# Optimization experiments

Measured on AMD Instinct MI355X. Metric: run time of the kernel, lower is better.

Reference implementation:

```python
import jax, jax.numpy as jnp
import numpy as np
import jax.scipy.special as jsp

N_RESERVOIR = 8192
N_INPUT = 64
N_LAYERS = 3
INPUT_SCALE = 0.4
RES_SCALE = 0.9
BIAS_SCALE = 0.1
ALPHA = 1.0  # activation_fn_args = (1.0,)
N_HADAMARD = 1 << int(np.ceil(np.log2(N_INPUT + N_RESERVOIR)))  # 16384
N_PADDING = N_HADAMARD - N_RESERVOIR - N_INPUT
BATCH = 512


def fwht(x):
    """Fast Walsh-Hadamard transform along last axis. x: [B, n], n a power of 2."""
    B, n = x.shape
    h = 1
    while h < n:
        x = x.reshape(B, n // (2 * h), 2, h)
        a = x[:, :, 0, :]
        b = x[:, :, 1, :]
        x = jnp.concatenate([a + b, a - b], axis=-1).reshape(B, n)
        h *= 2
    return x


def leaky_erf(x, state, alpha):
    return (1.0 - alpha) * state + alpha * jsp.erf(x)


def setup_inputs() -> dict:
    key = jax.random.key(0)
    k1, k2, k3, k4 = jax.random.split(key, 4)
    state = jax.random.normal(k1, (BATCH, N_RESERVOIR), dtype=jnp.float32)
    inputs = jax.random.normal(k2, (BATCH, N_INPUT), dtype=jnp.float32)
    bias = BIAS_SCALE * jax.random.normal(k3, (N_RESERVOIR,), dtype=jnp.float32)
    # structured-transform diagonals: random Rademacher signs, one per layer
    diag = jnp.where(jax.random.uniform(k4, (N_LAYERS, N_HADAMARD)) < 0.5, -1.0, 1.0).astype(jnp.float32)
    return {"state": state, "inputs": inputs, "bias": bias, "diag": diag}


def reference(state, inputs, bias, diag):
    B = state.shape[0]
    pad = jnp.zeros((B, N_PADDING), dtype=state.dtype)
    X = jnp.concatenate([RES_SCALE * state, INPUT_SCALE * inputs, pad], axis=1)  # [B, N_HADAMARD]
    for l in range(N_LAYERS):
        X = fwht(X * diag[l])
    z = X[:, :N_RESERVOIR] / N_HADAMARD + bias
    return leaky_erf(z, state, ALPHA)
```

## Files before the change

kernel.cpp:

```cpp
#include <hip/hip_runtime.h>
#include <math.h>

#define NH    16384
#define NRES  8192
#define NINP  64
#define BATCH 512

typedef float v2f __attribute__((ext_vector_type(2)));

__device__ __forceinline__ constexpr int gfoldc(int v) {
    return ((v >> 5) & 7) ^ ((v >> 8) & 7) ^ ((v >> 11) & 7);
}
__device__ __forceinline__ constexpr int physf(int v) { return v ^ (gfoldc(v) << 2); }

template <int T>
__device__ __forceinline__ void pstage(v2f X[32]) {
#pragma unroll
    for (int p = 0; p < 32; ++p) if (!(p & T)) {
        v2f A = X[p], B = X[p | T];
        X[p]     = A + B;
        X[p | T] = A - B;
    }
}
__device__ __forceinline__ void vstage0(v2f X[32]) {
#pragma unroll
    for (int p = 0; p < 32; ++p) {
        float a = X[p].x, b = X[p].y;
        X[p].x = a + b; X[p].y = a - b;
    }
}

template <int CTRL>
__device__ __forceinline__ float dppf(float v) {
    return __builtin_bit_cast(float,
        __builtin_amdgcn_update_dpp(0, __builtin_bit_cast(int, v), CTRL, 0xF, 0xF, true));
}
template <int CTRL>
__device__ __forceinline__ void dpp_bfly(v2f X[32], v2f sgn) {
#pragma unroll
    for (int p = 0; p < 32; ++p) {
        float y0 = dppf<CTRL>(X[p].x);
        float y1 = dppf<CTRL>(X[p].y);
        X[p] = sgn * X[p] + (v2f){y0, y1};
    }
}

__device__ __forceinline__ void pl16_swap(float& a, float& b) {
    asm("v_permlane16_swap_b32 %0, %1" : "+v"(a), "+v"(b));
}
__device__ __forceinline__ void pl32_swap(float& a, float& b) {
    asm("v_permlane32_swap_b32 %0, %1" : "+v"(a), "+v"(b));
}
__device__ __forceinline__ void swap_j2_l4(v2f X[32]) {
#pragma unroll
    for (int p = 0; p < 32; ++p) if (!(p & 8)) {
        float a = X[p].x, b = X[p | 8].x; pl16_swap(a, b); X[p].x = a; X[p | 8].x = b;
        float c = X[p].y, d = X[p | 8].y; pl16_swap(c, d); X[p].y = c; X[p | 8].y = d;
    }
}
__device__ __forceinline__ void swap_j3_l5(v2f X[32]) {
#pragma unroll
    for (int p = 0; p < 32; ++p) if (!(p & 16)) {
        float a = X[p].x, b = X[p | 16].x; pl32_swap(a, b); X[p].x = a; X[p | 16].x = b;
        float c = X[p].y, d = X[p | 16].y; pl32_swap(c, d); X[p].y = c; X[p | 16].y = d;
    }
}

#define GOFF4(g, G0, G1, G2, G3) \
    ((((g) & 1) ? (G0) : 0) | (((g) & 2) ? (G1) : 0) | \
     (((g) & 4) ? (G2) : 0) | (((g) & 8) ? (G3) : 0))

#define WRX(Q, G0, G1, G2, G3) do { _Pragma("unroll") \
    for (int g = 0; g < 16; ++g) { \
        const int a = (Q) ^ physf(GOFF4(g, G0, G1, G2, G3)); \
        lds4[(unsigned)a >> 2] = \
            make_float4(X[2*g].x, X[2*g].y, X[2*g+1].x, X[2*g+1].y); \
    } } while (0)

#define RDX(Q, G0, G1, G2, G3) do { _Pragma("unroll") \
    for (int g = 0; g < 16; ++g) { \
        const int a = (Q) ^ physf(GOFF4(g, G0, G1, G2, G3)); \
        float4 v = lds4[(unsigned)a >> 2]; \
        X[2*g]   = (v2f){v.x, v.y}; \
        X[2*g+1] = (v2f){v.z, v.w}; \
    } } while (0)

#define DIAG_LOAD(PF, BASE, G0, G1, G2, G3) do { _Pragma("unroll") \
    for (int g = 0; g < 16; ++g) \
        (PF)[g] = *(const float4*)((BASE) + GOFF4(g, G0, G1, G2, G3)); } while (0)

#define DIAG_APPLY(PF) do { _Pragma("unroll") \
    for (int g = 0; g < 16; ++g) { \
        X[2*g]   *= (v2f){(PF)[g].x, (PF)[g].y}; \
        X[2*g+1] *= (v2f){(PF)[g].z, (PF)[g].w}; \
    } } while (0)

#define BAR() asm volatile("s_waitcnt lgkmcnt(0)\n\ts_barrier" ::: "memory")

__device__ __forceinline__ float erf_fast(float z) {
    float p = z * z;
    float u = z * fmaf(p, 0.10090f, 1.1283793f);
    float e = __builtin_amdgcn_exp2f(u * 2.8853902f);
    float r = __builtin_amdgcn_rcpf(e + 1.0f);
    return fmaf(-2.0f, r, 1.0f);
}

__global__ __launch_bounds__(256, 2) void st_kernel(
    const float* __restrict__ state, const float* __restrict__ inputs,
    const float* __restrict__ bias,  const float* __restrict__ diag,
    float* __restrict__ out)
{
    __shared__ float4 lds4[NH / 4];
    const int t = threadIdx.x;
    const int r = blockIdx.x;
    const int l = t & 63, w = t >> 6;
    const int l0=l&1, l1=(l>>1)&1, l2=(l>>2)&1, l3=(l>>3)&1, l4=(l>>4)&1, l5=(l>>5)&1;
    const int w0=w&1, w1=(w>>1)&1;

    const v2f s1 = (v2f){l0 ? -1.f : 1.f, l0 ? -1.f : 1.f};
    const v2f s2 = (v2f){l1 ? -1.f : 1.f, l1 ? -1.f : 1.f};

    const int b_w1 = l0*64 + l1*128 + l2*256 + l3*512 + l4*16 + l5*32
                   + w0*4096 + w1*8192;
    const int b_r1 = l0*4 + l1*8 + l2*64 + l3*128 + l4*16 + l5*32
                   + w0*1024 + w1*2048;
    const int b_w2 = l0*4 + l1*8 + l2*64 + l3*128 + l4*4096 + l5*8192
                   + w0*1024 + w1*2048;
    const int b_r2 = l0*4 + l1*8 + l2*256 + l3*512 + l4*16 + l5*32
                   + w0*4096 + w1*8192;
    const int b_w3 = l0*4 + l1*8 + l2*256 + l3*512 + l4*1024 + l5*2048
                   + w0*4096 + w1*8192;

    v2f X[32];
    float4 pf[16];

    if (t < 128) {
        const float* srow = state + (size_t)r * NRES + t * 64;
        const float* d0   = diag + t * 64;
#pragma unroll
        for (int g = 0; g < 16; ++g) {
            float4 v = *(const float4*)(srow + 4 * g);
            float4 d = *(const float4*)(d0 + 4 * g);
            X[2*g]   = (v2f){0.9f * v.x * d.x, 0.9f * v.y * d.y};
            X[2*g+1] = (v2f){0.9f * v.z * d.z, 0.9f * v.w * d.w};
        }
    } else if (t == 128) {
        const float* irow = inputs + r * NINP;
        const float* d0   = diag + NRES;
#pragma unroll
        for (int g = 0; g < 16; ++g) {
            float4 v = *(const float4*)(irow + 4 * g);
            float4 d = *(const float4*)(d0 + 4 * g);
            X[2*g]   = (v2f){0.4f * v.x * d.x, 0.4f * v.y * d.y};
            X[2*g+1] = (v2f){0.4f * v.z * d.z, 0.4f * v.w * d.w};
        }
    } else {
#pragma unroll
        for (int p = 0; p < 32; ++p) X[p] = (v2f){0.f, 0.f};
    }

    vstage0(X); pstage<1>(X);
    pstage<2>(X); pstage<4>(X); pstage<8>(X); pstage<16>(X);
    dpp_bfly<0xB1>(X, s1);
    dpp_bfly<0x4E>(X, s2);
    swap_j2_l4(X); swap_j3_l5(X);
    pstage<8>(X); pstage<16>(X);

    DIAG_LOAD(pf, diag + NH + b_r1, 256, 512, 4096, 8192);

    { const int Q = physf(b_w1); WRX(Q, 4, 8, 1024, 2048); }
    BAR();
    { const int Q = physf(b_r1); RDX(Q, 256, 512, 4096, 8192); }
    pstage<2>(X); pstage<4>(X); pstage<8>(X); pstage<16>(X);

    DIAG_APPLY(pf);
    vstage0(X); pstage<1>(X);
    pstage<2>(X); pstage<4>(X); pstage<8>(X); pstage<16>(X);
    dpp_bfly<0xB1>(X, s1);
    dpp_bfly<0x4E>(X, s2);
    swap_j2_l4(X); swap_j3_l5(X);
    pstage<8>(X); pstage<16>(X);

    DIAG_LOAD(pf, diag + 2 * NH + b_r2, 64, 128, 1024, 2048);

    BAR();
    { const int Q = physf(b_w2); WRX(Q, 256, 512, 16, 32); }
    BAR();
    { const int Q = physf(b_r2); RDX(Q, 64, 128, 1024, 2048); }
    pstage<2>(X); pstage<4>(X); pstage<8>(X); pstage<16>(X);

    DIAG_APPLY(pf);
    vstage0(X); pstage<1>(X);
    pstage<2>(X); pstage<4>(X); pstage<8>(X); pstage<16>(X);
    dpp_bfly<0xB1>(X, s1);
    dpp_bfly<0x4E>(X, s2);
    swap_j2_l4(X); swap_j3_l5(X);
    pstage<8>(X); pstage<16>(X);

    float4 bv[8];
#pragma unroll
    for (int g = 0; g < 8; ++g)
        bv[g] = *(const float4*)(bias + b_r1 + GOFF4(g, 256, 512, 4096, 0));

    BAR();
    { const int Q = physf(b_w3); WRX(Q, 64, 128, 16, 32); }
    BAR();
    { const int Q = physf(b_r1); RDX(Q, 256, 512, 4096, 8192); }
    pstage<2>(X); pstage<4>(X); pstage<8>(X); pstage<16>(X);

    {
        float* orow = out + (size_t)r * NRES;
        const float inv = 1.0f / (float)NH;
#pragma unroll
        for (int g = 0; g < 8; ++g) {
            const int a = b_r1 + GOFF4(g, 256, 512, 4096, 0);
            float4 o;
            o.x = erf_fast(fmaf(X[2*g].x,   inv, bv[g].x));
            o.y = erf_fast(fmaf(X[2*g].y,   inv, bv[g].y));
            o.z = erf_fast(fmaf(X[2*g+1].x, inv, bv[g].z));
            o.w = erf_fast(fmaf(X[2*g+1].y, inv, bv[g].w));
            *(float4*)(orow + a) = o;
        }
    }
}

extern "C" void kernel_launch(void* const* d_in, const int* in_sizes, int n_in,
                              void* d_out, int out_size, void* d_ws, size_t ws_size,
                              hipStream_t stream) {
    (void)in_sizes; (void)n_in; (void)out_size; (void)d_ws; (void)ws_size;
    const float* state  = (const float*)d_in[0];
    const float* inputs = (const float*)d_in[1];
    const float* bias   = (const float*)d_in[2];
    const float* diag   = (const float*)d_in[3];
    float* out = (float*)d_out;

    hipLaunchKernelGGL(st_kernel, dim3(BATCH), dim3(256), 0, stream,
                       state, inputs, bias, diag, out);
}
```

Measured before the change: 23.70 us.

## Process two batch rows per block to share diag/bias loads and barriers

Each block now handles two batch rows, keeping two register-resident 16K-element vectors (XA, XB) and two LDS buffers, so diag and bias loads and barrier counts are amortized across rows and there is more independent work between synchronizations. The grid is halved to 256 blocks and launch bounds drop to one block per SIMD group. This roughly doubles register and LDS use per block (128 KB LDS), which cuts occupancy and leaves only 256 blocks on 256 CUs, with a risk of spills.

```diff
diff --git a/kernel.cpp b/kernel.cpp
--- a/kernel.cpp
+++ b/kernel.cpp
@@ -66,34 +66,53 @@
     }
 }
 
+__device__ __forceinline__ void phase_pre(v2f X[32], v2f s1, v2f s2) {
+    vstage0(X); pstage<1>(X);
+    pstage<2>(X); pstage<4>(X); pstage<8>(X); pstage<16>(X);
+    dpp_bfly<0xB1>(X, s1);
+    dpp_bfly<0x4E>(X, s2);
+    swap_j2_l4(X); swap_j3_l5(X);
+    pstage<8>(X); pstage<16>(X);
+}
+__device__ __forceinline__ void phase_post(v2f X[32]) {
+    pstage<2>(X); pstage<4>(X); pstage<8>(X); pstage<16>(X);
+}
+
 #define GOFF4(g, G0, G1, G2, G3) \
     ((((g) & 1) ? (G0) : 0) | (((g) & 2) ? (G1) : 0) | \
      (((g) & 4) ? (G2) : 0) | (((g) & 8) ? (G3) : 0))
 
-#define WRX(Q, G0, G1, G2, G3) do { _Pragma("unroll") \
-    for (int g = 0; g < 16; ++g) { \
-        const int a = (Q) ^ physf(GOFF4(g, G0, G1, G2, G3)); \
-        lds4[(unsigned)a >> 2] = \
-            make_float4(X[2*g].x, X[2*g].y, X[2*g+1].x, X[2*g+1].y); \
-    } } while (0)
-
-#define RDX(Q, G0, G1, G2, G3) do { _Pragma("unroll") \
-    for (int g = 0; g < 16; ++g) { \
-        const int a = (Q) ^ physf(GOFF4(g, G0, G1, G2, G3)); \
-        float4 v = lds4[(unsigned)a >> 2]; \
-        X[2*g]   = (v2f){v.x, v.y}; \
-        X[2*g+1] = (v2f){v.z, v.w}; \
-    } } while (0)
-
-#define DIAG_LOAD(PF, BASE, G0, G1, G2, G3) do { _Pragma("unroll") \
-    for (int g = 0; g < 16; ++g) \
-        (PF)[g] = *(const float4*)((BASE) + GOFF4(g, G0, G1, G2, G3)); } while (0)
-
-#define DIAG_APPLY(PF) do { _Pragma("unroll") \
-    for (int g = 0; g < 16; ++g) { \
-        X[2*g]   *= (v2f){(PF)[g].x, (PF)[g].y}; \
-        X[2*g+1] *= (v2f){(PF)[g].z, (PF)[g].w}; \
-    } } while (0)
+template <int G0, int G1, int G2, int G3>
+__device__ __forceinline__ void wrx(float4* L, int Q, const v2f X[32]) {
+#pragma unroll
+    for (int g = 0; g < 16; ++g) {
+        const int a = Q ^ physf(GOFF4(g, G0, G1, G2, G3));
+        L[(unsigned)a >> 2] = make_float4(X[2*g].x, X[2*g].y, X[2*g+1].x, X[2*g+1].y);
+    }
+}
+template <int G0, int G1, int G2, int G3>
+__device__ __forceinline__ void rdx(const float4* L, int Q, v2f X[32]) {
+#pragma unroll
+    for (int g = 0; g < 16; ++g) {
+        const int a = Q ^ physf(GOFF4(g, G0, G1, G2, G3));
+        float4 v = L[(unsigned)a >> 2];
+        X[2*g]   = (v2f){v.x, v.y};
+        X[2*g+1] = (v2f){v.z, v.w};
+    }
+}
+template <int G0, int G1, int G2, int G3>
+__device__ __forceinline__ void diag_load(float4 pf[16], const float* base) {
+#pragma unroll
+    for (int g = 0; g < 16; ++g)
+        pf[g] = *(const float4*)(base + GOFF4(g, G0, G1, G2, G3));
+}
+__device__ __forceinline__ void diag_apply(const float4 pf[16], v2f X[32]) {
+#pragma unroll
+    for (int g = 0; g < 16; ++g) {
+        X[2*g]   *= (v2f){pf[g].x, pf[g].y};
+        X[2*g+1] *= (v2f){pf[g].z, pf[g].w};
+    }
+}
 
 #define BAR() asm volatile("s_waitcnt lgkmcnt(0)\n\ts_barrier" ::: "memory")
 
@@ -105,14 +124,15 @@
     return fmaf(-2.0f, r, 1.0f);
 }
 
-__global__ __launch_bounds__(256, 2) void st_kernel(
+__global__ __launch_bounds__(256, 1) void st_kernel(
     const float* __restrict__ state, const float* __restrict__ inputs,
     const float* __restrict__ bias,  const float* __restrict__ diag,
     float* __restrict__ out)
 {
-    __shared__ float4 lds4[NH / 4];
+    __shared__ float4 lds4[2][NH / 4];
     const int t = threadIdx.x;
-    const int r = blockIdx.x;
+    const int rA = blockIdx.x * 2;
+    const int rB = rA + 1;
     const int l = t & 63, w = t >> 6;
     const int l0=l&1, l1=(l>>1)&1, l2=(l>>2)&1, l3=(l>>3)&1, l4=(l>>4)&1, l5=(l>>5)&1;
     const int w0=w&1, w1=(w>>1)&1;
@@ -131,71 +151,81 @@
     const int b_w3 = l0*4 + l1*8 + l2*256 + l3*512 + l4*1024 + l5*2048
                    + w0*4096 + w1*8192;
 
-    v2f X[32];
+    v2f XA[32], XB[32];
     float4 pf[16];
 
     if (t < 128) {
-        const float* srow = state + (size_t)r * NRES + t * 64;
-        const float* d0   = diag + t * 64;
+        const float* sA = state + (size_t)rA * NRES + t * 64;
+        const float* sB = state + (size_t)rB * NRES + t * 64;
+        const float* d0 = diag + t * 64;
 #pragma unroll
         for (int g = 0; g < 16; ++g) {
-            float4 v = *(const float4*)(srow + 4 * g);
+            float4 a = *(const float4*)(sA + 4 * g);
+            float4 b = *(const float4*)(sB + 4 * g);
             float4 d = *(const float4*)(d0 + 4 * g);
-            X[2*g]   = (v2f){0.9f * v.x * d.x, 0.9f * v.y * d.y};
-            X[2*g+1] = (v2f){0.9f * v.z * d.z, 0.9f * v.w * d.w};
+            XA[2*g]   = (v2f){0.9f * a.x * d.x, 0.9f * a.y * d.y};
+            XA[2*g+1] = (v2f){0.9f * a.z * d.z, 0.9f * a.w * d.w};
+            XB[2*g]   = (v2f){0.9f * b.x * d.x, 0.9f * b.y * d.y};
+            XB[2*g+1] = (v2f){0.9f * b.z * d.z, 0.9f * b.w * d.w};
         }
     } else if (t == 128) {
-        const float* irow = inputs + r * NINP;
-        const float* d0   = diag + NRES;
+        const float* iA = inputs + rA * NINP;
+        const float* iB = inputs + rB * NINP;
+        const float* d0 = diag + NRES;
 #pragma unroll
         for (int g = 0; g < 16; ++g) {
-            float4 v = *(const float4*)(irow + 4 * g);
+            float4 a = *(const float4*)(iA + 4 * g);
+            float4 b = *(const float4*)(iB + 4 * g);
             float4 d = *(const float4*)(d0 + 4 * g);
-            X[2*g]   = (v2f){0.4f * v.x * d.x, 0.4f * v.y * d.y};
-            X[2*g+1] = (v2f){0.4f * v.z * d.z, 0.4f * v.w * d.w};
+            XA[2*g]   = (v2f){0.4f * a.x * d.x, 0.4f * a.y * d.y};
+            XA[2*g+1] = (v2f){0.4f * a.z * d.z, 0.4f * a.w * d.w};
+            XB[2*g]   = (v2f){0.4f * b.x * d.x, 0.4f * b.y * d.y};
+            XB[2*g+1] = (v2f){0.4f * b.z * d.z, 0.4f * b.w * d.w};
         }
     } else {
 #pragma unroll
-        for (int p = 0; p < 32; ++p) X[p] = (v2f){0.f, 0.f};
-    }
-
-    vstage0(X); pstage<1>(X);
-    pstage<2>(X); pstage<4>(X); pstage<8>(X); pstage<16>(X);
-    dpp_bfly<0xB1>(X, s1);
-    dpp_bfly<0x4E>(X, s2);
-    swap_j2_l4(X); swap_j3_l5(X);
-    pstage<8>(X); pstage<16>(X);
-
-    DIAG_LOAD(pf, diag + NH + b_r1, 256, 512, 4096, 8192);
-
-    { const int Q = physf(b_w1); WRX(Q, 4, 8, 1024, 2048); }
+        for (int p = 0; p < 32; ++p) { XA[p] = (v2f){0.f, 0.f}; XB[p] = (v2f){0.f, 0.f}; }
+    }
+
+    phase_pre(XA, s1, s2);
+    phase_pre(XB, s1, s2);
+
+    diag_load<256, 512, 4096, 8192>(pf, diag + NH + b_r1);
+
+    {
+        const int Qw = physf(b_w1), Qr = physf(b_r1);
+        wrx<4, 8, 1024, 2048>(lds4[0], Qw, XA);
+        wrx<4, 8, 1024, 2048>(lds4[1], Qw, XB);
+        BAR();
+        rdx<256, 512, 4096, 8192>(lds4[0], Qr, XA);
+        rdx<256, 512, 4096, 8192>(lds4[1], Qr, XB);
+    }
+    phase_post(XA);
+    phase_post(XB);
+
+    diag_apply(pf, XA);
+    diag_apply(pf, XB);
+    phase_pre(XA, s1, s2);
+    phase_pre(XB, s1, s2);
+
+    diag_load<64, 128, 1024, 2048>(pf, diag + 2 * NH + b_r2);
+
     BAR();
-    { const int Q = physf(b_r1); RDX(Q, 256, 512, 4096, 8192); }
-    pstage<2>(X); pstage<4>(X); pstage<8>(X); pstage<16>(X);
-
-    DIAG_APPLY(pf);
-    vstage0(X); pstage<1>(X);
-    pstage<2>(X); pstage<4>(X); pstage<8>(X); pstage<16>(X);
-    dpp_bfly<0xB1>(X, s1);
-    dpp_bfly<0x4E>(X, s2);
-    swap_j2_l4(X); swap_j3_l5(X);
-    pstage<8>(X); pstage<16>(X);
-
-    DIAG_LOAD(pf, diag + 2 * NH + b_r2, 64, 128, 1024, 2048);
-
-    BAR();
-    { const int Q = physf(b_w2); WRX(Q, 256, 512, 16, 32); }
-    BAR();
-    { const int Q = physf(b_r2); RDX(Q, 64, 128, 1024, 2048); }
-    pstage<2>(X); pstage<4>(X); pstage<8>(X); pstage<16>(X);
-
-    DIAG_APPLY(pf);
-    vstage0(X); pstage<1>(X);
-    pstage<2>(X); pstage<4>(X); pstage<8>(X); pstage<16>(X);
-    dpp_bfly<0xB1>(X, s1);
-    dpp_bfly<0x4E>(X, s2);
-    swap_j2_l4(X); swap_j3_l5(X);
-    pstage<8>(X); pstage<16>(X);
+    {
+        const int Qw = physf(b_w2), Qr = physf(b_r2);
+        wrx<256, 512, 16, 32>(lds4[0], Qw, XA);
+        wrx<256, 512, 16, 32>(lds4[1], Qw, XB);
+        BAR();
+        rdx<64, 128, 1024, 2048>(lds4[0], Qr, XA);
+        rdx<64, 128, 1024, 2048>(lds4[1], Qr, XB);
+    }
+    phase_post(XA);
+    phase_post(XB);
+
+    diag_apply(pf, XA);
+    diag_apply(pf, XB);
+    phase_pre(XA, s1, s2);
+    phase_pre(XB, s1, s2);
 
     float4 bv[8];
 #pragma unroll
@@ -203,23 +233,35 @@
         bv[g] = *(const float4*)(bias + b_r1 + GOFF4(g, 256, 512, 4096, 0));
 
     BAR();
-    { const int Q = physf(b_w3); WRX(Q, 64, 128, 16, 32); }
-    BAR();
-    { const int Q = physf(b_r1); RDX(Q, 256, 512, 4096, 8192); }
-    pstage<2>(X); pstage<4>(X); pstage<8>(X); pstage<16>(X);
-
-    {
-        float* orow = out + (size_t)r * NRES;
+    {
+        const int Qw = physf(b_w3), Qr = physf(b_r1);
+        wrx<64, 128, 16, 32>(lds4[0], Qw, XA);
+        wrx<64, 128, 16, 32>(lds4[1], Qw, XB);
+        BAR();
+        rdx<256, 512, 4096, 8192>(lds4[0], Qr, XA);
+        rdx<256, 512, 4096, 8192>(lds4[1], Qr, XB);
+    }
+    phase_post(XA);
+    phase_post(XB);
+
+    {
+        float* oA = out + (size_t)rA * NRES;
+        float* oB = out + (size_t)rB * NRES;
         const float inv = 1.0f / (float)NH;
 #pragma unroll
         for (int g = 0; g < 8; ++g) {
             const int a = b_r1 + GOFF4(g, 256, 512, 4096, 0);
-            float4 o;
-            o.x = erf_fast(fmaf(X[2*g].x,   inv, bv[g].x));
-            o.y = erf_fast(fmaf(X[2*g].y,   inv, bv[g].y));
-            o.z = erf_fast(fmaf(X[2*g+1].x, inv, bv[g].z));
-            o.w = erf_fast(fmaf(X[2*g+1].y, inv, bv[g].w));
-            *(float4*)(orow + a) = o;
+            float4 oa, ob;
+            oa.x = erf_fast(fmaf(XA[2*g].x,   inv, bv[g].x));
+            oa.y = erf_fast(fmaf(XA[2*g].y,   inv, bv[g].y));
+            oa.z = erf_fast(fmaf(XA[2*g+1].x, inv, bv[g].z));
+            oa.w = erf_fast(fmaf(XA[2*g+1].y, inv, bv[g].w));
+            ob.x = erf_fast(fmaf(XB[2*g].x,   inv, bv[g].x));
+            ob.y = erf_fast(fmaf(XB[2*g].y,   inv, bv[g].y));
+            ob.z = erf_fast(fmaf(XB[2*g+1].x, inv, bv[g].z));
+            ob.w = erf_fast(fmaf(XB[2*g+1].y, inv, bv[g].w));
+            *(float4*)(oA + a) = oa;
+            *(float4*)(oB + a) = ob;
         }
     }
 }
@@ -234,6 +276,6 @@
     const float* diag   = (const float*)d_in[3];
     float* out = (float*)d_out;
 
-    hipLaunchKernelGGL(st_kernel, dim3(BATCH), dim3(256), 0, stream,
+    hipLaunchKernelGGL(st_kernel, dim3(BATCH / 2), dim3(256), 0, stream,
                        state, inputs, bias, diag, out);
 }
```

Result: slower. 26.74 us (+12.8%).
